# Kernel tuning notes

Hardware: AMD Instinct MI355X
Metric: run time of the kernel (lower is better)

## Reference

```python
import jax, jax.numpy as jnp
import numpy as np

B, A, C, H, W = 64, 3, 80, 76, 76  # batch, masked anchors, classes, grid h, grid w
# anchors [12,16,19,36,40,28] / stride(8) * scale(1.0)
ANCHORS = jnp.array([[1.5, 2.0], [2.375, 4.5], [5.0, 3.5]], dtype=jnp.float32)  # [A, 2] (w, h)
SCALE_XY = 1.0


def setup_inputs() -> dict:
    key = jax.random.key(0)
    output = jax.random.normal(key, (B, A * (5 + C), H, W), dtype=jnp.float32)
    return {"output": output}


def reference(output):
    b, _, h, w = output.shape
    o = output.reshape(b, A, 5 + C, h, w)
    # box center offsets: sigmoid * scale_x_y - 0.5*(scale_x_y - 1)
    bxy = jax.nn.sigmoid(o[:, :, 0:2]) * SCALE_XY - 0.5 * (SCALE_XY - 1.0)  # [b,A,2,h,w]
    bwh = jnp.exp(o[:, :, 2:4])                                             # scaled=False -> exp
    det = jax.nn.sigmoid(o[:, :, 4])                                        # [b,A,h,w]
    cls = jax.nn.sigmoid(o[:, :, 5:])                                       # [b,A,C,h,w]

    gx = jnp.arange(w, dtype=jnp.float32)[None, None, None, :]  # grid_x over width
    gy = jnp.arange(h, dtype=jnp.float32)[None, None, :, None]  # grid_y over height
    bx = (bxy[:, :, 0] + gx) / w                                  # [b,A,h,w], normalized
    by = (bxy[:, :, 1] + gy) / h
    bw = bwh[:, :, 0] * ANCHORS[None, :, 0, None, None] / w
    bh = bwh[:, :, 1] * ANCHORS[None, :, 1, None, None] / h

    n = A * h * w
    bx = bx.reshape(b, n, 1)
    by = by.reshape(b, n, 1)
    bw = bw.reshape(b, n, 1)
    bh = bh.reshape(b, n, 1)
    bx1 = bx - bw * 0.5
    by1 = by - bh * 0.5
    boxes = jnp.concatenate([bx1, by1, bx1 + bw, by1 + bh], axis=2).reshape(b, n, 1, 4)

    # cls_confs permuted to [b, A*h*w, C] then scaled by objectness
    confs = cls.transpose(0, 1, 3, 4, 2).reshape(b, n, C) * det.reshape(b, n, 1)
    return boxes, confs
```

## Files before the change

kernel.cpp:

```cpp
#include <hip/hip_runtime.h>


#define Bn 64
#define An 3
#define Cn 80
#define Hn 76
#define Wn 76
#define HW (Hn * Wn)
#define Nn (An * HW)
#define CHn (5 + Cn)
#define Rr 2
#define ROWLEN (Rr * Wn)
#define PITCH 153
#define BOX_TOTAL (Bn * Nn * 4)
#define NWG (Bn * An * (Hn / Rr))
#define CPX (NWG / 8)
#define NT4 (CHn * (ROWLEN / 4))
#define NCONF (ROWLEN * Cn)

typedef float floatx4 __attribute__((ext_vector_type(4)));

__device__ __forceinline__ float sigmoidf_(float x) {
    return 1.0f / (1.0f + __expf(-x));
}

__launch_bounds__(512)
__global__ void yolo_kernel(const float* __restrict__ in, float* __restrict__ out) {
    __shared__ float s_in[CHn * PITCH];
    __shared__ float s_det[ROWLEN];

    const int raw = blockIdx.x;
    const int bid = (raw & 7) * CPX + (raw >> 3);

    const int yb = bid % (Hn / Rr);
    const int t  = bid / (Hn / Rr);
    const int a  = t % An;
    const int b  = t / An;
    const int y0 = yb * Rr;

    const float aw = (a == 0) ? 1.5f : ((a == 1) ? 2.375f : 5.0f);
    const float ah = (a == 0) ? 2.0f : ((a == 1) ? 4.5f   : 3.5f);

    const int tid = threadIdx.x;
    const float* __restrict__ src =
        in + ((size_t)(b * (An * CHn) + a * CHn)) * HW + (size_t)y0 * Wn;

    for (int i = tid; i < NT4; i += 512) {
        const int ch = i / (ROWLEN / 4);
        const int q  = i % (ROWLEN / 4);
        const float4 v = *(const float4*)(src + (size_t)ch * HW + q * 4);
        float* d = &s_in[ch * PITCH + q * 4];
        d[0] = v.x; d[1] = v.y; d[2] = v.z; d[3] = v.w;
    }
    __syncthreads();

    const int n_base = a * HW + y0 * Wn;

    if (tid < ROWLEN) {
        const int x  = (tid < Wn) ? tid : tid - Wn;
        const int yy = y0 + ((tid < Wn) ? 0 : 1);
        const float sx  = sigmoidf_(s_in[0 * PITCH + tid]);
        const float sy  = sigmoidf_(s_in[1 * PITCH + tid]);
        const float ew  = __expf(s_in[2 * PITCH + tid]);
        const float eh  = __expf(s_in[3 * PITCH + tid]);
        const float det = sigmoidf_(s_in[4 * PITCH + tid]);
        s_det[tid] = det;

        const float bx = (sx + (float)x) * (1.0f / Wn);
        const float by = (sy + (float)yy) * (1.0f / Hn);
        const float bw = ew * aw * (1.0f / Wn);
        const float bh = eh * ah * (1.0f / Hn);
        const float bx1 = bx - 0.5f * bw;
        const float by1 = by - 0.5f * bh;

        const size_t n = (size_t)b * Nn + n_base + tid;
        floatx4 box;
        box.x = bx1; box.y = by1; box.z = bx1 + bw; box.w = by1 + bh;
        __builtin_nontemporal_store(box, (floatx4*)(out + n * 4));
    }
    __syncthreads();

    float* __restrict__ confs = out + BOX_TOTAL + ((size_t)b * Nn + n_base) * Cn;
    for (int i = tid; i < NCONF; i += 512) {
        const int s = i / Cn;
        const int c = i % Cn;
        const float v = sigmoidf_(s_in[(5 + c) * PITCH + s]) * s_det[s];
        __builtin_nontemporal_store(v, confs + i);
    }
}

extern "C" void kernel_launch(void* const* d_in, const int* in_sizes, int n_in,
                              void* d_out, int out_size, void* d_ws, size_t ws_size,
                              hipStream_t stream) {
    (void)in_sizes; (void)n_in; (void)d_ws; (void)ws_size; (void)out_size;
    const float* in = (const float*)d_in[0];
    float* out = (float*)d_out;
    yolo_kernel<<<NWG, 512, 0, stream>>>(in, out);
}
```

Baseline: 143.6 us.

## Stage sigmoid channels as bf16 in LDS to double rows per block

The kernel now rounds the class, objectness and xy-offset channels to bf16 before storing them in shared memory. Only the width/height channels stay fp32. Halving their footprint lets each workgroup process four grid rows instead of two within roughly the same shared memory, which halves the number of workgroups and spreads per-block overhead over more work. The cost is reduced precision on the sigmoid inputs and on the stored objectness, plus extra conversion arithmetic on the load path.

```diff
diff --git a/kernel.cpp b/kernel.cpp
--- a/kernel.cpp
+++ b/kernel.cpp
@@ -9,9 +9,10 @@
 #define HW (Hn * Wn)
 #define Nn (An * HW)
 #define CHn (5 + Cn)
-#define Rr 2
+#define Rr 4
 #define ROWLEN (Rr * Wn)
-#define PITCH 153
+#define PITCH_S 308
+#define PITCH_W 304
 #define BOX_TOTAL (Bn * Nn * 4)
 #define NWG (Bn * An * (Hn / Rr))
 #define CPX (NWG / 8)
@@ -24,10 +25,19 @@
     return 1.0f / (1.0f + __expf(-x));
 }
 
+__device__ __forceinline__ unsigned short f2bf(float f) {
+    unsigned u = __float_as_uint(f);
+    return (unsigned short)((u + 0x7FFFu + ((u >> 16) & 1u)) >> 16);
+}
+__device__ __forceinline__ float bf2f(unsigned short h) {
+    return __uint_as_float(((unsigned)h) << 16);
+}
+
 __launch_bounds__(512)
 __global__ void yolo_kernel(const float* __restrict__ in, float* __restrict__ out) {
-    __shared__ float s_in[CHn * PITCH];
-    __shared__ float s_det[ROWLEN];
+    __shared__ unsigned short s_sig[83 * PITCH_S];
+    __shared__ float          s_wh[2 * PITCH_W];
+    __shared__ unsigned short s_det[ROWLEN];
 
     const int raw = blockIdx.x;
     const int bid = (raw & 7) * CPX + (raw >> 3);
@@ -49,22 +59,29 @@
         const int ch = i / (ROWLEN / 4);
         const int q  = i % (ROWLEN / 4);
         const float4 v = *(const float4*)(src + (size_t)ch * HW + q * 4);
-        float* d = &s_in[ch * PITCH + q * 4];
-        d[0] = v.x; d[1] = v.y; d[2] = v.z; d[3] = v.w;
+        if (ch == 2 || ch == 3) {
+            float* d = &s_wh[(ch - 2) * PITCH_W + q * 4];
+            d[0] = v.x; d[1] = v.y; d[2] = v.z; d[3] = v.w;
+        } else {
+            const int row = (ch < 2) ? ch : ((ch == 4) ? 2 : 3 + (ch - 5));
+            ushort4 h;
+            h.x = f2bf(v.x); h.y = f2bf(v.y); h.z = f2bf(v.z); h.w = f2bf(v.w);
+            *(ushort4*)&s_sig[row * PITCH_S + q * 4] = h;
+        }
     }
     __syncthreads();
 
     const int n_base = a * HW + y0 * Wn;
 
     if (tid < ROWLEN) {
-        const int x  = (tid < Wn) ? tid : tid - Wn;
-        const int yy = y0 + ((tid < Wn) ? 0 : 1);
-        const float sx  = sigmoidf_(s_in[0 * PITCH + tid]);
-        const float sy  = sigmoidf_(s_in[1 * PITCH + tid]);
-        const float ew  = __expf(s_in[2 * PITCH + tid]);
-        const float eh  = __expf(s_in[3 * PITCH + tid]);
-        const float det = sigmoidf_(s_in[4 * PITCH + tid]);
-        s_det[tid] = det;
+        const int x  = tid % Wn;
+        const int yy = y0 + tid / Wn;
+        const float sx  = sigmoidf_(bf2f(s_sig[0 * PITCH_S + tid]));
+        const float sy  = sigmoidf_(bf2f(s_sig[1 * PITCH_S + tid]));
+        const float ew  = __expf(s_wh[0 * PITCH_W + tid]);
+        const float eh  = __expf(s_wh[1 * PITCH_W + tid]);
+        const float det = sigmoidf_(bf2f(s_sig[2 * PITCH_S + tid]));
+        s_det[tid] = f2bf(det);
 
         const float bx = (sx + (float)x) * (1.0f / Wn);
         const float by = (sy + (float)yy) * (1.0f / Hn);
@@ -84,7 +101,7 @@
     for (int i = tid; i < NCONF; i += 512) {
         const int s = i / Cn;
         const int c = i % Cn;
-        const float v = sigmoidf_(s_in[(5 + c) * PITCH + s]) * s_det[s];
+        const float v = sigmoidf_(bf2f(s_sig[(3 + c) * PITCH_S + s])) * bf2f(s_det[s]);
         __builtin_nontemporal_store(v, confs + i);
     }
 }
```

New measurement: 159.3 us. +10.9%, slower.
